# Kernel tuning notes

Hardware: AMD Instinct MI355X
Metric: run time of the kernel (lower is better)

Reference implementation:

```python
import jax, jax.numpy as jnp
import numpy as np

D_MODEL = 768
D_STATE = 16
D_CONV = 4
EXPAND = 2
D_INNER = EXPAND * D_MODEL  # 1536
BATCH = 2
SEQLEN = 4096


def setup_inputs() -> dict:
    key = jax.random.key(0)
    ks = jax.random.split(key, 8)
    s = 0.02
    return {
        "hidden_states": jax.random.normal(ks[0], (BATCH, SEQLEN, D_MODEL), jnp.float32),
        "W_in": jax.random.normal(ks[1], (D_MODEL, 2 * D_INNER), jnp.float32) * s,
        "conv_w": jax.random.normal(ks[2], (D_INNER, 1, D_CONV), jnp.float32) * s,
        "conv_b": jnp.zeros((D_INNER,), jnp.float32),
        "W_x": jax.random.normal(ks[3], (D_INNER, 2 * D_STATE + D_INNER), jnp.float32) * s,
        "W_dt": jax.random.normal(ks[4], (D_INNER, D_INNER), jnp.float32) * s,
        "b_dt": jnp.zeros((D_INNER,), jnp.float32),
        "A_log": jax.random.uniform(ks[5], (D_INNER, D_STATE), jnp.float32, minval=-1.0, maxval=0.0),
        "D": jnp.ones((D_INNER,), jnp.float32),
        "W_out": jax.random.normal(ks[6], (D_INNER, D_MODEL), jnp.float32) * s,
    }


def _silu(x):
    return x * jax.nn.sigmoid(x)


def reference(hidden_states, W_in, conv_w, conv_b, W_x, W_dt, b_dt, A_log, D, W_out):
    B, L, _ = hidden_states.shape
    # in_proj and split into x / gate z  (torch splits first half -> x, second -> z)
    xz = hidden_states @ W_in                      # (B, L, 2*ed)
    x, z = xz[..., :D_INNER], xz[..., D_INNER:]
    # causal depthwise conv1d (torch pads d_conv-1 both sides then truncates to L == left pad)
    xc = jnp.swapaxes(x, 1, 2)                     # (B, ed, L)
    xc = jax.lax.conv_general_dilated(
        xc, conv_w, window_strides=(1,), padding=[(D_CONV - 1, 0)],
        dimension_numbers=("NCH", "OIH", "NCH"), feature_group_count=D_INNER)
    x = jnp.swapaxes(xc, 1, 2) + conv_b            # (B, L, ed)
    x = _silu(x)
    # input-dependent SSM params
    xp = x @ W_x                                   # (B, L, 2*ds + ed)
    Bm = jax.nn.softmax(xp[..., :D_STATE], axis=-1)          # (B, L, ds)
    Cm = xp[..., D_STATE:2 * D_STATE]                          # (B, L, ds)
    delta = jax.nn.softplus(xp[..., 2 * D_STATE:] @ W_dt + b_dt)  # (B, L, ed)
    A = -jnp.exp(A_log.astype(jnp.float32))        # (ed, ds)

    def step(h, t):
        dt, Bt, Ct, ut = t                         # (B,ed),(B,ds),(B,ds),(B,ed)
        dA = jnp.exp(dt[:, :, None] * A)           # (B, ed, ds)
        h = dA * h + (dt[:, :, None] * Bt[:, None, :]) * ut[:, :, None]
        y = jnp.einsum('bs,bds->bd', Ct, h)        # (B, ed)
        return h, y

    h0 = jnp.zeros((B, D_INNER, D_STATE), x.dtype)
    ts = (jnp.swapaxes(delta, 0, 1), jnp.swapaxes(Bm, 0, 1),
          jnp.swapaxes(Cm, 0, 1), jnp.swapaxes(x, 0, 1))
    _, ys = jax.lax.scan(step, h0, ts)             # ys: (L, B, ed)
    y = jnp.swapaxes(ys, 0, 1)                     # (B, L, ed)
    # gating + out projection (torch fallback path does NOT add D * u)
    y = y * _silu(z)
    return y @ W_out
```

## Files before the change

kernel.cpp:

```cpp
#include <hip/hip_runtime.h>
#include <hip/hip_bf16.h>
#include <math.h>

#define D_MODEL 768
#define D_STATE 16
#define D_CONVW 4
#define D_INNER 1536
#define BATCH   2
#define SEQLEN  4096
#define NROWS   (BATCH*SEQLEN)
#define NCHUNK  128
#define LCHUNK  (SEQLEN/NCHUNK)

typedef __attribute__((ext_vector_type(8))) short short8;
typedef __attribute__((ext_vector_type(4))) float floatx4;

__device__ inline unsigned short f2b(float x) {
    unsigned u = __float_as_uint(x);
    return (unsigned short)((u + 0x7fffu + ((u >> 16) & 1u)) >> 16);
}
__device__ inline float b2f(unsigned short b) {
    return __uint_as_float(((unsigned)b) << 16);
}

#define GLDS(gp, lp) __builtin_amdgcn_global_load_lds( \
    (const __attribute__((address_space(1))) void*)(gp), \
    (__attribute__((address_space(3))) void*)(lp), 16, 0, 0)


template<int EPI, int OUTBF16>
__global__ __launch_bounds__(512, 4) void gemm_w8(
    const unsigned short* __restrict__ A, int lda,
    const unsigned short* __restrict__ Bt, int ldb,
    void* __restrict__ Cv, int ldc, float* __restrict__ C2,
    int N, int K, const float* __restrict__ bias, int nbx)
{
    __shared__ unsigned short As0[256*32], As1[256*32];
    __shared__ unsigned short Bs0[128*32], Bs1[128*32];

    const int nwg = gridDim.x;
    const int cpx = nwg >> 3;
    const int wg  = blockIdx.x;
    const int xcd = wg & 7, local = wg >> 3;
    int bmi, bni;
    if ((cpx % nbx == 0) && ((nbx & 1) == 0)) {
        const int R   = cpx / nbx;
        const int p   = local / (2 * R);
        const int idx = local % (2 * R);
        bmi = xcd * R + (idx >> 1);
        bni = p * 2 + (idx & 1);
    } else {
        const int swz = xcd * cpx + local;
        bmi = swz / nbx;
        bni = swz % nbx;
    }
    const int bm = bmi * 256;
    const int bn = bni * 128;

    const int tid  = threadIdx.x;
    const int lane = tid & 63;
    const int wave = tid >> 6;
    const int wm   = (wave >> 1) * 64;
    const int wn   = (wave & 1) * 64;
    const int l15  = lane & 15;
    const int lg   = lane >> 4;

    const int sr    = tid >> 2;
    const int sg    = ((tid & 3) ^ ((tid >> 3) & 3)) * 8;
    const int lbase = (tid & ~63) * 16;

    const unsigned short* pa0 = A  + (size_t)(bm + sr) * lda + sg;
    const unsigned short* pa1 = A  + (size_t)(bm + 128 + sr) * lda + sg;
    const unsigned short* pb0 = Bt + (size_t)(bn + sr) * ldb + sg;

    int aoff[4], boff[4];
    #pragma unroll
    for (int i = 0; i < 4; ++i) {
        const int tr = wm + i * 16 + l15;
        aoff[i] = tr * 64 + ((lg ^ ((tr >> 1) & 3)) << 4);
    }
    #pragma unroll
    for (int j = 0; j < 4; ++j) {
        const int tr = wn + j * 16 + l15;
        boff[j] = tr * 64 + ((lg ^ ((tr >> 1) & 3)) << 4);
    }

    floatx4 acc[4][4] = {};

    auto stage = [&](unsigned short (&SA)[256*32], unsigned short (&SB)[128*32]) {
        GLDS(pa0, (char*)SA + lbase);
        GLDS(pa1, (char*)SA + 8192 + lbase);
        GLDS(pb0, (char*)SB + lbase);
        pa0 += 32; pa1 += 32; pb0 += 32;
    };

    auto compute = [&](const unsigned short (&CA)[256*32],
                       const unsigned short (&CB)[128*32]) {
        short8 af[4], bfv[4];
        #pragma unroll
        for (int i = 0; i < 4; ++i)
            af[i] = *(const short8*)((const char*)&CA[0] + aoff[i]);
        #pragma unroll
        for (int j = 0; j < 4; ++j)
            bfv[j] = *(const short8*)((const char*)&CB[0] + boff[j]);
        #pragma unroll
        for (int i = 0; i < 4; ++i)
            #pragma unroll
            for (int j = 0; j < 4; ++j)
                acc[i][j] = __builtin_amdgcn_mfma_f32_16x16x32_bf16(
                    af[i], bfv[j], acc[i][j], 0, 0, 0);
    };

    const int NT = K >> 5;

    stage(As0, Bs0);

    #define STEP(SA, SB, CA, CB, T)                                          \
    {                                                                        \
        if ((T) + 1 < NT) {                                                  \
            stage(SA, SB);                                                   \
            asm volatile("s_waitcnt vmcnt(3)" ::: "memory");                 \
        } else {                                                             \
            asm volatile("s_waitcnt vmcnt(0)" ::: "memory");                 \
        }                                                                    \
        __builtin_amdgcn_sched_barrier(0);                                   \
        __builtin_amdgcn_s_barrier();                                        \
        __builtin_amdgcn_sched_barrier(0);                                   \
        compute(CA, CB);                                                     \
        __builtin_amdgcn_sched_barrier(0);                                   \
        __builtin_amdgcn_s_barrier();                                        \
        __builtin_amdgcn_sched_barrier(0);                                   \
    }

    for (int t = 0; t < NT; t += 2) {
        STEP(As1, Bs1, As0, Bs0, t);
        STEP(As0, Bs0, As1, Bs1, t + 1);
    }
    #undef STEP

    #pragma unroll
    for (int i = 0; i < 4; ++i) {
        #pragma unroll
        for (int r = 0; r < 4; ++r) {
            const int gm = bm + wm + i * 16 + lg * 4 + r;
            #pragma unroll
            for (int j = 0; j < 4; ++j) {
                const int gn = bn + wn + j * 16 + l15;
                float v = acc[i][j][r];
                if (EPI == 3) {
                    if (gn < 32) {
                        C2[(size_t)gm * 32 + gn] = v;
                    } else if (gn < N) {
                        v += bias[gn - 32];
                        v = (v > 20.f) ? v : log1pf(__expf(v));
                        ((unsigned short*)Cv)[(size_t)gm * 1536 + gn - 32] = f2b(v);
                    }
                } else {
                    if (gn < N) {
                        if (OUTBF16)
                            ((unsigned short*)Cv)[(size_t)gm * ldc + gn] = f2b(v);
                        else
                            ((float*)Cv)[(size_t)gm * ldc + gn] = v;
                    }
                }
            }
        }
    }
}

template<int EPI, int OUTBF16>
__global__ __launch_bounds__(256, 4) void gemm_p2(
    const unsigned short* __restrict__ A, int lda,
    const unsigned short* __restrict__ Bt, int ldb,
    void* __restrict__ Cv, int ldc, float* __restrict__ C2,
    int N, int K, const float* __restrict__ bias, int nbx)
{
    __shared__ unsigned short As0[128*32], As1[128*32];
    __shared__ unsigned short Bs0[128*32], Bs1[128*32];

    const int nwg = gridDim.x;
    const int cpx = nwg >> 3;
    const int wg  = blockIdx.x;
    const int xcd = wg & 7, local = wg >> 3;
    int bmi, bni;
    if ((cpx % nbx == 0) && ((nbx & 1) == 0)) {
        const int R   = cpx / nbx;
        const int p   = local / (2 * R);
        const int idx = local % (2 * R);
        bmi = xcd * R + (idx >> 1);
        bni = p * 2 + (idx & 1);
    } else {
        const int swz = xcd * cpx + local;
        bmi = swz / nbx;
        bni = swz % nbx;
    }
    const int bm = bmi * 128;
    const int bn = bni * 128;

    const int tid  = threadIdx.x;
    const int lane = tid & 63;
    const int wave = tid >> 6;
    const int wm   = (wave >> 1) * 64;
    const int wn   = (wave & 1) * 64;
    const int l15  = lane & 15;
    const int lg   = lane >> 4;

    const int sr    = tid >> 2;
    const int sg    = ((tid & 3) ^ ((tid >> 3) & 3)) * 8;
    const int lbase = (tid & ~63) * 16;

    const unsigned short* pa0 = A  + (size_t)(bm + sr) * lda + sg;
    const unsigned short* pa1 = A  + (size_t)(bm + 64 + sr) * lda + sg;
    const unsigned short* pb0 = Bt + (size_t)(bn + sr) * ldb + sg;
    const unsigned short* pb1 = Bt + (size_t)(bn + 64 + sr) * ldb + sg;

    int aoff[4], boff[4];
    #pragma unroll
    for (int i = 0; i < 4; ++i) {
        const int tr = wm + i * 16 + l15;
        aoff[i] = tr * 64 + ((lg ^ ((tr >> 1) & 3)) << 4);
    }
    #pragma unroll
    for (int j = 0; j < 4; ++j) {
        const int tr = wn + j * 16 + l15;
        boff[j] = tr * 64 + ((lg ^ ((tr >> 1) & 3)) << 4);
    }

    floatx4 acc[4][4] = {};

    auto stage = [&](unsigned short (&SA)[128*32], unsigned short (&SB)[128*32]) {
        GLDS(pa0, (char*)SA + lbase);
        GLDS(pa1, (char*)SA + 4096 + lbase);
        GLDS(pb0, (char*)SB + lbase);
        GLDS(pb1, (char*)SB + 4096 + lbase);
        pa0 += 32; pa1 += 32; pb0 += 32; pb1 += 32;
    };

    auto compute = [&](const unsigned short (&CA)[128*32],
                       const unsigned short (&CB)[128*32]) {
        short8 af[4], bfv[4];
        #pragma unroll
        for (int i = 0; i < 4; ++i)
            af[i] = *(const short8*)((const char*)&CA[0] + aoff[i]);
        #pragma unroll
        for (int j = 0; j < 4; ++j)
            bfv[j] = *(const short8*)((const char*)&CB[0] + boff[j]);
        #pragma unroll
        for (int i = 0; i < 4; ++i)
            #pragma unroll
            for (int j = 0; j < 4; ++j)
                acc[i][j] = __builtin_amdgcn_mfma_f32_16x16x32_bf16(
                    af[i], bfv[j], acc[i][j], 0, 0, 0);
    };

    const int NT = K >> 5;

    stage(As0, Bs0);

    #define STEP(SA, SB, CA, CB, T)                                          \
    {                                                                        \
        if ((T) + 1 < NT) {                                                  \
            stage(SA, SB);                                                   \
            asm volatile("s_waitcnt vmcnt(4)" ::: "memory");                 \
        } else {                                                             \
            asm volatile("s_waitcnt vmcnt(0)" ::: "memory");                 \
        }                                                                    \
        __builtin_amdgcn_sched_barrier(0);                                   \
        __builtin_amdgcn_s_barrier();                                        \
        __builtin_amdgcn_sched_barrier(0);                                   \
        compute(CA, CB);                                                     \
        __builtin_amdgcn_sched_barrier(0);                                   \
        __builtin_amdgcn_s_barrier();                                        \
        __builtin_amdgcn_sched_barrier(0);                                   \
    }

    for (int t = 0; t < NT; t += 2) {
        STEP(As1, Bs1, As0, Bs0, t);
        STEP(As0, Bs0, As1, Bs1, t + 1);
    }
    #undef STEP

    #pragma unroll
    for (int i = 0; i < 4; ++i) {
        #pragma unroll
        for (int r = 0; r < 4; ++r) {
            const int gm = bm + wm + i * 16 + lg * 4 + r;
            #pragma unroll
            for (int j = 0; j < 4; ++j) {
                const int gn = bn + wn + j * 16 + l15;
                float v = acc[i][j][r];
                if (gn < N) {
                    if (OUTBF16)
                        ((unsigned short*)Cv)[(size_t)gm * ldc + gn] = f2b(v);
                    else
                        ((float*)Cv)[(size_t)gm * ldc + gn] = v;
                }
            }
        }
    }
}

__global__ __launch_bounds__(256) void transpose_bf16(
    const float* __restrict__ W, unsigned short* __restrict__ Wt, int K, int N)
{
    __shared__ float t[32][33];
    const int nt = blockIdx.x * 32, kt = blockIdx.y * 32;
    const int tx = threadIdx.x & 31, ty = threadIdx.x >> 5;
    #pragma unroll
    for (int r = 0; r < 4; ++r) {
        const int k = ty + r * 8;
        const int n = nt + tx;
        float v = 0.f;
        if (n < N) v = W[(size_t)(kt + k) * N + n];
        t[k][tx] = v;
    }
    __syncthreads();
    #pragma unroll
    for (int r = 0; r < 4; ++r) {
        const int nl = ty + r * 8;
        Wt[(size_t)(nt + nl) * K + kt + tx] = f2b(t[tx][nl]);
    }
}

__global__ __launch_bounds__(256) void f32_to_bf16(
    const float* __restrict__ in, unsigned short* __restrict__ o, int n4)
{
    const int i = blockIdx.x * 256 + threadIdx.x;
    if (i >= n4) return;
    float4 v = ((const float4*)in)[i];
    ushort4 r;
    r.x = f2b(v.x); r.y = f2b(v.y); r.z = f2b(v.z); r.w = f2b(v.w);
    ((ushort4*)o)[i] = r;
}

__global__ __launch_bounds__(256) void wx32_to_bf16(
    const float* __restrict__ Wx, unsigned short* __restrict__ o)
{
    const int i = blockIdx.x * 256 + threadIdx.x;
    if (i >= 1536 * 384) return;
    const int row = i / 384, q = i % 384;
    float4 v = *(const float4*)(Wx + (size_t)row * 1568 + 32 + q * 4);
    ushort4 r;
    r.x = f2b(v.x); r.y = f2b(v.y); r.z = f2b(v.z); r.w = f2b(v.w);
    *(ushort4*)(o + (size_t)row * 1536 + q * 4) = r;
}

__global__ __launch_bounds__(256) void conv_silu4r(
    const unsigned short* __restrict__ xzb, const float* __restrict__ w,
    const float* __restrict__ cb, unsigned short* __restrict__ ub)
{
    const int i = blockIdx.x * 256 + threadIdx.x;
    if (i >= (NROWS / 4) * 192) return;
    const int g    = i % 192;
    const int rowq = i / 192;
    const int row0 = rowq * 4;
    const int lb   = row0 % SEQLEN;
    const int d0   = g * 8;

    float4 we[8];
    float  cbv[8];
    #pragma unroll
    for (int e = 0; e < 8; ++e) {
        we[e]  = *(const float4*)&w[(d0 + e) * 4];
        cbv[e] = cb[d0 + e];
    }

    short8 xr[7];
    #pragma unroll
    for (int k = 0; k < 7; ++k) {
        const int ll = lb - 3 + k;
        if (ll >= 0)
            xr[k] = *(const short8*)&xzb[(size_t)(row0 - 3 + k) * 3072 + d0];
        else
            xr[k] = short8{0,0,0,0,0,0,0,0};
    }

    #pragma unroll
    for (int r = 0; r < 4; ++r) {
        unsigned short o[8];
        #pragma unroll
        for (int e = 0; e < 8; ++e) {
            float a = cbv[e];
            a = fmaf(b2f((unsigned short)xr[r + 0][e]), we[e].x, a);
            a = fmaf(b2f((unsigned short)xr[r + 1][e]), we[e].y, a);
            a = fmaf(b2f((unsigned short)xr[r + 2][e]), we[e].z, a);
            a = fmaf(b2f((unsigned short)xr[r + 3][e]), we[e].w, a);
            o[e] = f2b(a / (1.f + __expf(-a)));
        }
        *(short8*)&ub[(size_t)(row0 + r) * 1536 + d0] = *(short8*)o;
    }
}

__global__ __launch_bounds__(256) void softmax_bc_kernel(
    const float* __restrict__ xp32, float* __restrict__ Bsm, float* __restrict__ Csm)
{
    const int row = blockIdx.x * 256 + threadIdx.x;
    if (row >= NROWS) return;
    const float* p = xp32 + (size_t)row * 32;
    float v[16];
    #pragma unroll
    for (int q = 0; q < 4; ++q) {
        float4 t = *(const float4*)(p + q * 4);
        v[q*4+0]=t.x; v[q*4+1]=t.y; v[q*4+2]=t.z; v[q*4+3]=t.w;
    }
    float mx = v[0];
    #pragma unroll
    for (int s = 1; s < 16; ++s) mx = fmaxf(mx, v[s]);
    float sum = 0.f;
    #pragma unroll
    for (int s = 0; s < 16; ++s) { v[s] = __expf(v[s] - mx); sum += v[s]; }
    const float inv = 1.f / sum;
    float* bo = Bsm + (size_t)row * 16;
    float* co = Csm + (size_t)row * 16;
    #pragma unroll
    for (int s = 0; s < 16; ++s) bo[s] = v[s] * inv;
    #pragma unroll
    for (int q = 0; q < 4; ++q)
        *(float4*)(co + q * 4) = *(const float4*)(p + 16 + q * 4);
}

__global__ __launch_bounds__(256) void scan_chunk_state(
    const unsigned short* __restrict__ deltab, const unsigned short* __restrict__ ub,
    const float* __restrict__ Bsm, const float* __restrict__ A_log,
    float* __restrict__ chunkS, float* __restrict__ dtsum)
{
    const int gid = blockIdx.x * 256 + threadIdx.x;
    const int d = gid % D_INNER;
    const int c = (gid / D_INNER) % NCHUNK;
    const int b = gid / (D_INNER * NCHUNK);

    float A2[16];
    #pragma unroll
    for (int q = 0; q < 4; ++q) {
        float4 t = *(const float4*)(A_log + d * 16 + q * 4);
        A2[q*4+0] = -__expf(t.x) * 1.44269504089f;
        A2[q*4+1] = -__expf(t.y) * 1.44269504089f;
        A2[q*4+2] = -__expf(t.z) * 1.44269504089f;
        A2[q*4+3] = -__expf(t.w) * 1.44269504089f;
    }
    float h[16];
    #pragma unroll
    for (int s = 0; s < 16; ++s) h[s] = 0.f;
    float dts = 0.f;

    const int t0 = c * LCHUNK;
    for (int t = t0; t < t0 + LCHUNK; ++t) {
        const size_t rowoff = (size_t)b * SEQLEN + t;
        const float dt = b2f(deltab[rowoff * D_INNER + d]);
        const float uu = b2f(ub[rowoff * D_INNER + d]);
        const float du = dt * uu;
        dts += dt;
        const float4* Bp = (const float4*)(Bsm + rowoff * 16);
        float Bv[16];
        #pragma unroll
        for (int q = 0; q < 4; ++q) {
            float4 tb = Bp[q];
            Bv[q*4+0]=tb.x; Bv[q*4+1]=tb.y; Bv[q*4+2]=tb.z; Bv[q*4+3]=tb.w;
        }
        #pragma unroll
        for (int s = 0; s < 16; ++s) {
            const float dA = exp2f(dt * A2[s]);
            h[s] = fmaf(dA, h[s], du * Bv[s]);
        }
    }
    float* S = chunkS + (size_t)gid * 16;
    #pragma unroll
    for (int q = 0; q < 4; ++q)
        *(float4*)(S + q * 4) = make_float4(h[q*4+0], h[q*4+1], h[q*4+2], h[q*4+3]);
    dtsum[gid] = dts;
}

__global__ __launch_bounds__(256) void scan_chunk_scan(
    const float* __restrict__ A_log, const float* __restrict__ dtsum,
    float* __restrict__ chunkS)
{
    const int gid = blockIdx.x * 256 + threadIdx.x;
    if (gid >= BATCH * D_INNER * 16) return;
    const int s = gid % 16;
    const int d = (gid / 16) % D_INNER;
    const int b = gid / (16 * D_INNER);
    const float A2 = -__expf(A_log[d * 16 + s]) * 1.44269504089f;
    float hprev = 0.f;
    for (int c = 0; c < NCHUNK; ++c) {
        const size_t cidx = ((size_t)(b * NCHUNK + c) * D_INNER + d);
        const float P  = exp2f(A2 * dtsum[cidx]);
        const size_t idx = cidx * 16 + s;
        const float Sc = chunkS[idx];
        chunkS[idx] = hprev;
        hprev = fmaf(P, hprev, Sc);
    }
}

__global__ __launch_bounds__(256) void scan_output(
    const unsigned short* __restrict__ deltab, const unsigned short* __restrict__ ub,
    const float* __restrict__ Bsm, const float* __restrict__ Csm,
    const float* __restrict__ A_log, const float* __restrict__ chunkS,
    const unsigned short* __restrict__ xzb, unsigned short* __restrict__ yb)
{
    const int gid = blockIdx.x * 256 + threadIdx.x;
    const int d = gid % D_INNER;
    const int c = (gid / D_INNER) % NCHUNK;
    const int b = gid / (D_INNER * NCHUNK);

    float A2[16];
    #pragma unroll
    for (int q = 0; q < 4; ++q) {
        float4 t = *(const float4*)(A_log + d * 16 + q * 4);
        A2[q*4+0] = -__expf(t.x) * 1.44269504089f;
        A2[q*4+1] = -__expf(t.y) * 1.44269504089f;
        A2[q*4+2] = -__expf(t.z) * 1.44269504089f;
        A2[q*4+3] = -__expf(t.w) * 1.44269504089f;
    }
    float h[16];
    const float* S = chunkS + (size_t)gid * 16;
    #pragma unroll
    for (int q = 0; q < 4; ++q) {
        float4 t = *(const float4*)(S + q * 4);
        h[q*4+0]=t.x; h[q*4+1]=t.y; h[q*4+2]=t.z; h[q*4+3]=t.w;
    }

    const int t0 = c * LCHUNK;
    for (int t = t0; t < t0 + LCHUNK; ++t) {
        const size_t rowoff = (size_t)b * SEQLEN + t;
        const float dt = b2f(deltab[rowoff * D_INNER + d]);
        const float uu = b2f(ub[rowoff * D_INNER + d]);
        const float du = dt * uu;
        const float4* Bp = (const float4*)(Bsm + rowoff * 16);
        const float4* Cp = (const float4*)(Csm + rowoff * 16);
        float Bv[16], Cv[16];
        #pragma unroll
        for (int q = 0; q < 4; ++q) {
            float4 tb = Bp[q], tc = Cp[q];
            Bv[q*4+0]=tb.x; Bv[q*4+1]=tb.y; Bv[q*4+2]=tb.z; Bv[q*4+3]=tb.w;
            Cv[q*4+0]=tc.x; Cv[q*4+1]=tc.y; Cv[q*4+2]=tc.z; Cv[q*4+3]=tc.w;
        }
        float yv = 0.f;
        #pragma unroll
        for (int s = 0; s < 16; ++s) {
            const float dA = exp2f(dt * A2[s]);
            h[s] = fmaf(dA, h[s], du * Bv[s]);
            yv = fmaf(Cv[s], h[s], yv);
        }
        const float z = b2f(xzb[rowoff * (2 * D_INNER) + D_INNER + d]);
        const float sz = z / (1.f + __expf(-z));
        yb[rowoff * D_INNER + d] = f2b(yv * sz);
    }
}

extern "C" void kernel_launch(void* const* d_in, const int* in_sizes, int n_in,
                              void* d_out, int out_size, void* d_ws, size_t ws_size,
                              hipStream_t stream)
{
    const float* hs     = (const float*)d_in[0];
    const float* W_in   = (const float*)d_in[1];
    const float* conv_w = (const float*)d_in[2];
    const float* conv_b = (const float*)d_in[3];
    const float* W_x    = (const float*)d_in[4];
    const float* W_dt   = (const float*)d_in[5];
    const float* b_dt   = (const float*)d_in[6];
    const float* A_log  = (const float*)d_in[7];
    const float* W_out  = (const float*)d_in[9];
    float* out = (float*)d_out;

    char* w = (char*)d_ws;
    auto alloc = [&](size_t bytes) { char* p = w; w += (bytes + 255) & ~(size_t)255; return p; };
    float*          xp32   = (float*)alloc((size_t)NROWS * 32 * 4);
    unsigned short* deltab = (unsigned short*)alloc((size_t)NROWS * 1536 * 2);
    float*          Bsm    = (float*)alloc((size_t)NROWS * 16 * 4);
    float*          Csm    = (float*)alloc((size_t)NROWS * 16 * 4);
    float*          chunkS = (float*)alloc((size_t)BATCH * NCHUNK * D_INNER * 16 * 4);
    float*          dtsum  = (float*)alloc((size_t)BATCH * NCHUNK * D_INNER * 4);
    unsigned short* xzb    = (unsigned short*)alloc((size_t)NROWS * 3072 * 2);
    unsigned short* ub     = (unsigned short*)alloc((size_t)NROWS * 1536 * 2);
    unsigned short* yb     = (unsigned short*)alloc((size_t)NROWS * 1536 * 2);
    unsigned short* hsb    = (unsigned short*)alloc((size_t)NROWS * 768 * 2);
    unsigned short* Wt_in  = (unsigned short*)alloc((size_t)3072 * 768 * 2);
    unsigned short* Wt_x   = (unsigned short*)alloc((size_t)1792 * 1536 * 2);
    unsigned short* Wt_dt  = (unsigned short*)alloc((size_t)1536 * 1536 * 2);
    unsigned short* Wt_out = (unsigned short*)alloc((size_t)768 * 1536 * 2);
    unsigned short* wxb    = (unsigned short*)alloc((size_t)1536 * 1536 * 2);

    const dim3 blk(256);

    transpose_bf16<<<dim3(3072/32, 768/32),  blk, 0, stream>>>(W_in,  Wt_in,  768,  3072);
    transpose_bf16<<<dim3(1792/32, 1536/32), blk, 0, stream>>>(W_x,   Wt_x,   1536, 1568);
    transpose_bf16<<<dim3(1536/32, 1536/32), blk, 0, stream>>>(W_dt,  Wt_dt,  1536, 1536);
    transpose_bf16<<<dim3(768/32,  1536/32), blk, 0, stream>>>(W_out, Wt_out, 1536, 768);
    f32_to_bf16<<<(NROWS*768/4 + 255)/256, blk, 0, stream>>>(hs, hsb, NROWS*768/4);
    wx32_to_bf16<<<(1536*384 + 255)/256, blk, 0, stream>>>(W_x, wxb);

    gemm_p2<0,1><<<dim3(144), blk, 0, stream>>>(
        Wt_dt, 1536, wxb, 1536, Wt_x + (size_t)32 * 1536, 1536, nullptr,
        1536, 1536, nullptr, 12);

    gemm_w8<0,1><<<dim3(768), dim3(512), 0, stream>>>(
        hsb, 768, Wt_in, 768, xzb, 3072, nullptr, 3072, 768, nullptr, 24);

    conv_silu4r<<<((NROWS/4)*192)/256, blk, 0, stream>>>(xzb, conv_w, conv_b, ub);

    gemm_w8<3,0><<<dim3(416), dim3(512), 0, stream>>>(
        ub, 1536, Wt_x, 1536, deltab, 1536, xp32, 1568, 1536, b_dt, 13);

    softmax_bc_kernel<<<NROWS/256, blk, 0, stream>>>(xp32, Bsm, Csm);

    scan_chunk_state<<<(BATCH*NCHUNK*D_INNER)/256, blk, 0, stream>>>(
        deltab, ub, Bsm, A_log, chunkS, dtsum);
    scan_chunk_scan<<<(BATCH*D_INNER*16 + 255)/256, blk, 0, stream>>>(
        A_log, dtsum, chunkS);
    scan_output<<<(BATCH*NCHUNK*D_INNER)/256, blk, 0, stream>>>(
        deltab, ub, Bsm, Csm, A_log, chunkS, xzb, yb);

    gemm_p2<0,0><<<dim3(384), blk, 0, stream>>>(
        yb, 1536, Wt_out, 1536, out, 768, nullptr, 768, 1536, nullptr, 6);
}
```

Baseline: 444.7 us.

## Merge weight transposes, conversions, and two independent GEMMs into fewer launches

Combines the four weight transpose kernels into one launch and the two fp32-to-bf16 conversions into another. It also runs the W_dt·W_x weight-fusion GEMM and the input projection GEMM as a single grid, splitting blocks by index and sharing the 256x128 tile body. This removes several kernel launches and lets the small weight GEMM overlap with the large one instead of underfilling the device alone. The small GEMM switches from the 128-tile p2 kernel to the 256x128 w8 tile, which gives it fewer blocks.

```diff
diff --git a/kernel.cpp b/kernel.cpp
--- a/kernel.cpp
+++ b/kernel.cpp
@@ -29,18 +29,16 @@
 
 
 template<int EPI, int OUTBF16>
-__global__ __launch_bounds__(512, 4) void gemm_w8(
+__device__ __forceinline__ void gemm_w8_body(
+    int wg, int nwg,
+    unsigned short (&As0)[256*32], unsigned short (&As1)[256*32],
+    unsigned short (&Bs0)[128*32], unsigned short (&Bs1)[128*32],
     const unsigned short* __restrict__ A, int lda,
     const unsigned short* __restrict__ Bt, int ldb,
     void* __restrict__ Cv, int ldc, float* __restrict__ C2,
     int N, int K, const float* __restrict__ bias, int nbx)
 {
-    __shared__ unsigned short As0[256*32], As1[256*32];
-    __shared__ unsigned short Bs0[128*32], Bs1[128*32];
-
-    const int nwg = gridDim.x;
     const int cpx = nwg >> 3;
-    const int wg  = blockIdx.x;
     const int xcd = wg & 7, local = wg >> 3;
     int bmi, bni;
     if ((cpx % nbx == 0) && ((nbx & 1) == 0)) {
@@ -87,7 +85,11 @@
 
     floatx4 acc[4][4] = {};
 
-    auto stage = [&](unsigned short (&SA)[256*32], unsigned short (&SB)[128*32]) {
+    auto stage = [&]() {
+    };
+    (void)stage;
+
+    auto stageTo = [&](unsigned short (&SA)[256*32], unsigned short (&SB)[128*32]) {
         GLDS(pa0, (char*)SA + lbase);
         GLDS(pa1, (char*)SA + 8192 + lbase);
         GLDS(pb0, (char*)SB + lbase);
@@ -113,12 +115,12 @@
 
     const int NT = K >> 5;
 
-    stage(As0, Bs0);
-
-    #define STEP(SA, SB, CA, CB, T)                                          \
+    stageTo(As0, Bs0);
+
+    #define STEP_W8(SA, SB, CA, CB, T)                                       \
     {                                                                        \
         if ((T) + 1 < NT) {                                                  \
-            stage(SA, SB);                                                   \
+            stageTo(SA, SB);                                                 \
             asm volatile("s_waitcnt vmcnt(3)" ::: "memory");                 \
         } else {                                                             \
             asm volatile("s_waitcnt vmcnt(0)" ::: "memory");                 \
@@ -133,10 +135,10 @@
     }
 
     for (int t = 0; t < NT; t += 2) {
-        STEP(As1, Bs1, As0, Bs0, t);
-        STEP(As0, Bs0, As1, Bs1, t + 1);
-    }
-    #undef STEP
+        STEP_W8(As1, Bs1, As0, Bs0, t);
+        STEP_W8(As0, Bs0, As1, Bs1, t + 1);
+    }
+    #undef STEP_W8
 
     #pragma unroll
     for (int i = 0; i < 4; ++i) {
@@ -169,6 +171,38 @@
 }
 
 template<int EPI, int OUTBF16>
+__global__ __launch_bounds__(512, 4) void gemm_w8(
+    const unsigned short* __restrict__ A, int lda,
+    const unsigned short* __restrict__ Bt, int ldb,
+    void* __restrict__ Cv, int ldc, float* __restrict__ C2,
+    int N, int K, const float* __restrict__ bias, int nbx)
+{
+    __shared__ unsigned short As0[256*32], As1[256*32];
+    __shared__ unsigned short Bs0[128*32], Bs1[128*32];
+    gemm_w8_body<EPI, OUTBF16>(blockIdx.x, gridDim.x, As0, As1, Bs0, Bs1,
+                               A, lda, Bt, ldb, Cv, ldc, C2, N, K, bias, nbx);
+}
+
+__global__ __launch_bounds__(512, 4) void gemm_dual(
+    const unsigned short* __restrict__ Wt_dt, const unsigned short* __restrict__ wxb,
+    unsigned short* __restrict__ wtx32,
+    const unsigned short* __restrict__ hsb, const unsigned short* __restrict__ Wt_in,
+    unsigned short* __restrict__ xzb)
+{
+    __shared__ unsigned short As0[256*32], As1[256*32];
+    __shared__ unsigned short Bs0[128*32], Bs1[128*32];
+    if (blockIdx.x < 72) {
+        gemm_w8_body<0, 1>(blockIdx.x, 72, As0, As1, Bs0, Bs1,
+                           Wt_dt, 1536, wxb, 1536, wtx32, 1536, nullptr,
+                           1536, 1536, nullptr, 12);
+    } else {
+        gemm_w8_body<0, 1>(blockIdx.x - 72, 768, As0, As1, Bs0, Bs1,
+                           hsb, 768, Wt_in, 768, xzb, 3072, nullptr,
+                           3072, 768, nullptr, 24);
+    }
+}
+
+template<int EPI, int OUTBF16>
 __global__ __launch_bounds__(256, 4) void gemm_p2(
     const unsigned short* __restrict__ A, int lda,
     const unsigned short* __restrict__ Bt, int ldb,
@@ -300,11 +334,21 @@
     }
 }
 
-__global__ __launch_bounds__(256) void transpose_bf16(
-    const float* __restrict__ W, unsigned short* __restrict__ Wt, int K, int N)
-{
+__global__ __launch_bounds__(256) void transpose_all(
+    const float* __restrict__ W_in,  unsigned short* __restrict__ Wt_in,
+    const float* __restrict__ W_x,   unsigned short* __restrict__ Wt_x,
+    const float* __restrict__ W_dt,  unsigned short* __restrict__ Wt_dt,
+    const float* __restrict__ W_out, unsigned short* __restrict__ Wt_out)
+{
+    const int b = blockIdx.x;
+    const float* W; unsigned short* Wt; int K, N, nbx, lb;
+    if (b < 2304)      { W = W_in;  Wt = Wt_in;  K = 768;  N = 3072; nbx = 96; lb = b; }
+    else if (b < 4992) { W = W_x;   Wt = Wt_x;   K = 1536; N = 1568; nbx = 56; lb = b - 2304; }
+    else if (b < 7296) { W = W_dt;  Wt = Wt_dt;  K = 1536; N = 1536; nbx = 48; lb = b - 4992; }
+    else               { W = W_out; Wt = Wt_out; K = 1536; N = 768;  nbx = 24; lb = b - 7296; }
+    const int nt = (lb % nbx) * 32, kt = (lb / nbx) * 32;
+
     __shared__ float t[32][33];
-    const int nt = blockIdx.x * 32, kt = blockIdx.y * 32;
     const int tx = threadIdx.x & 31, ty = threadIdx.x >> 5;
     #pragma unroll
     for (int r = 0; r < 4; ++r) {
@@ -322,27 +366,27 @@
     }
 }
 
-__global__ __launch_bounds__(256) void f32_to_bf16(
-    const float* __restrict__ in, unsigned short* __restrict__ o, int n4)
-{
-    const int i = blockIdx.x * 256 + threadIdx.x;
-    if (i >= n4) return;
-    float4 v = ((const float4*)in)[i];
-    ushort4 r;
-    r.x = f2b(v.x); r.y = f2b(v.y); r.z = f2b(v.z); r.w = f2b(v.w);
-    ((ushort4*)o)[i] = r;
-}
-
-__global__ __launch_bounds__(256) void wx32_to_bf16(
-    const float* __restrict__ Wx, unsigned short* __restrict__ o)
-{
-    const int i = blockIdx.x * 256 + threadIdx.x;
-    if (i >= 1536 * 384) return;
-    const int row = i / 384, q = i % 384;
-    float4 v = *(const float4*)(Wx + (size_t)row * 1568 + 32 + q * 4);
-    ushort4 r;
-    r.x = f2b(v.x); r.y = f2b(v.y); r.z = f2b(v.z); r.w = f2b(v.w);
-    *(ushort4*)(o + (size_t)row * 1536 + q * 4) = r;
+__global__ __launch_bounds__(256) void convert_all(
+    const float* __restrict__ hs, unsigned short* __restrict__ hsb,
+    const float* __restrict__ Wx, unsigned short* __restrict__ wxb)
+{
+    const int NH = NROWS * 768 / 4;
+    int i = blockIdx.x * 256 + threadIdx.x;
+    if (i < NH) {
+        float4 v = ((const float4*)hs)[i];
+        ushort4 r;
+        r.x = f2b(v.x); r.y = f2b(v.y); r.z = f2b(v.z); r.w = f2b(v.w);
+        ((ushort4*)hsb)[i] = r;
+    } else {
+        i -= NH;
+        if (i < 1536 * 384) {
+            const int row = i / 384, q = i % 384;
+            float4 v = *(const float4*)(Wx + (size_t)row * 1568 + 32 + q * 4);
+            ushort4 r;
+            r.x = f2b(v.x); r.y = f2b(v.y); r.z = f2b(v.z); r.w = f2b(v.w);
+            *(ushort4*)(wxb + (size_t)row * 1536 + q * 4) = r;
+        }
+    }
 }
 
 __global__ __launch_bounds__(256) void conv_silu4r(
@@ -582,19 +626,12 @@
 
     const dim3 blk(256);
 
-    transpose_bf16<<<dim3(3072/32, 768/32),  blk, 0, stream>>>(W_in,  Wt_in,  768,  3072);
-    transpose_bf16<<<dim3(1792/32, 1536/32), blk, 0, stream>>>(W_x,   Wt_x,   1536, 1568);
-    transpose_bf16<<<dim3(1536/32, 1536/32), blk, 0, stream>>>(W_dt,  Wt_dt,  1536, 1536);
-    transpose_bf16<<<dim3(768/32,  1536/32), blk, 0, stream>>>(W_out, Wt_out, 1536, 768);
-    f32_to_bf16<<<(NROWS*768/4 + 255)/256, blk, 0, stream>>>(hs, hsb, NROWS*768/4);
-    wx32_to_bf16<<<(1536*384 + 255)/256, blk, 0, stream>>>(W_x, wxb);
-
-    gemm_p2<0,1><<<dim3(144), blk, 0, stream>>>(
-        Wt_dt, 1536, wxb, 1536, Wt_x + (size_t)32 * 1536, 1536, nullptr,
-        1536, 1536, nullptr, 12);
-
-    gemm_w8<0,1><<<dim3(768), dim3(512), 0, stream>>>(
-        hsb, 768, Wt_in, 768, xzb, 3072, nullptr, 3072, 768, nullptr, 24);
+    transpose_all<<<dim3(8448), blk, 0, stream>>>(
+        W_in, Wt_in, W_x, Wt_x, W_dt, Wt_dt, W_out, Wt_out);
+    convert_all<<<dim3(8448), blk, 0, stream>>>(hs, hsb, W_x, wxb);
+
+    gemm_dual<<<dim3(840), dim3(512), 0, stream>>>(
+        Wt_dt, wxb, Wt_x + (size_t)32 * 1536, hsb, Wt_in, xzb);
 
     conv_silu4r<<<((NROWS/4)*192)/256, blk, 0, stream>>>(xzb, conv_w, conv_b, ub);
 
```

Measured after the change: 408.8 us. -8.1%, faster.
